# Kernel optimization log

Measured on AMD Instinct MI355X. Metric: run time of the kernel, lower is better.

## Reference

```python
import jax, jax.numpy as jnp
import numpy as np

N_CLASSES = 5
N_SAMPLES = 512
D_EMB = 512


def setup_inputs() -> dict:
    key = jax.random.key(0)
    k1, k2, k3 = jax.random.split(key, 3)
    prediction = jax.random.normal(k1, (N_SAMPLES, D_EMB), dtype=jnp.float32)
    target = jax.random.randint(k2, (N_SAMPLES,), 0, N_CLASSES)
    # learnable_map=None -> all learnable, init = inverse_softplus(0.5 + 0.5*U[0,1))
    t = 0.5 + 0.5 * jax.random.uniform(k3, (N_CLASSES - 1,), dtype=jnp.float32)
    distances_raw = jnp.log(jnp.exp(t) - 1.0)  # inverse softplus (t < 20 always)
    return {"prediction": prediction, "distances_raw": distances_raw, "target": target}


def reference(prediction, distances_raw, target):
    n = prediction.shape[0]
    eps = 1e-8  # torch F.cosine_similarity eps
    xn = prediction / jnp.maximum(jnp.linalg.norm(prediction, axis=1, keepdims=True), eps)
    cos = xn @ xn.T  # [i, j] pairwise cosine similarity

    same = target[:, None] == target[None, :]          # label_diff <= 0
    positives = same & ~jnp.eye(n, dtype=bool)          # same label, not self
    negatives = ~same                                   # different label

    # ordinal class positions from softplus-parameterized gaps
    pos_d = jax.nn.softplus(distances_raw)
    class_pos = jnp.concatenate([jnp.zeros(1, dtype=pos_d.dtype), jnp.cumsum(pos_d)])
    cp = class_pos[target]
    margins = jnp.where(negatives, jnp.abs(cp[:, None] - cp[None, :]), 0.0)  # [i, j]

    # Original loop over anchor-positive columns k:
    #   n_pair_loss[k][i, j] = -cos[i, k] + cos[i, j] + margins[i, j]
    #   valid iff positives[i, k] and negatives[i, j]; invalid -> relu(-inf)=0
    base = cos + margins                                # [i, j]
    diff = base[:, None, :] - cos[:, :, None]           # [i, k, j]
    val = jnp.where(negatives[:, None, :], jax.nn.relu(diff), 0.0)
    s = jnp.where(positives, val.sum(axis=2), 0.0)      # [i, k]
    negcount = negatives.sum(axis=1)                    # [i]
    cnt = jnp.where(positives, negcount[:, None], 0)    # loss_mask2
    L = s / jnp.maximum(cnt, 1)                         # per (anchor i, positive k)

    # mean over nonzero entries (mean_n_pair_loss[mean_n_pair_loss != 0].mean())
    nz = (L != 0.0).sum()
    return L.sum() / jnp.maximum(nz, 1).astype(L.dtype)
```

## Files before the change

### kernel.cpp

```cpp
#include <hip/hip_runtime.h>
#include <math.h>

#define NS 512
#define DE 512
#define NCL 5
#define NBLK 256


__global__ __launch_bounds__(512, 2) void k_gram(const float* __restrict__ pred,
                                                 float* __restrict__ cosmat) {
    const int b  = blockIdx.x;
    const int ga = b >> 2;
    const int q  = b & 3;
    const int a0 = ga * 8;
    const int j0 = q * 128;

    const int tid  = threadIdx.x;
    const int w    = tid >> 6, lane = tid & 63;
    const int g    = lane >> 5;
    const int s    = lane & 31;

    const float4* p4 = (const float4*)pred;

    float4 fr[8][4];
#pragma unroll
    for (int a = 0; a < 8; a++) {
        const float4* pa = p4 + (size_t)(a0 + a) * (DE / 4);
#pragma unroll
        for (int p = 0; p < 4; p++) fr[a][p] = pa[p * 32 + s];
    }

    float rnA[8];
#pragma unroll
    for (int a = 0; a < 8; a++) {
        float aS = 0.0f;
#pragma unroll
        for (int p = 0; p < 4; p++) {
            float4 x = fr[a][p];
            aS = fmaf(x.x, x.x, aS); aS = fmaf(x.y, x.y, aS);
            aS = fmaf(x.z, x.z, aS); aS = fmaf(x.w, x.w, aS);
        }
#pragma unroll
        for (int m = 1; m <= 16; m <<= 1) aS += __shfl_xor(aS, m);
        rnA[a] = 1.0f / fmaxf(sqrtf(aS), 1e-8f);
    }

    const float4* rj0 = p4 + (size_t)(j0 + w * 16 + g) * (DE / 4);
    const int rstep = 2 * (DE / 4);
    float4 x0[4], x1[4];
#pragma unroll
    for (int p = 0; p < 4; p++) x0[p] = rj0[p * 32 + s];
#pragma unroll
    for (int p = 0; p < 4; p++) x1[p] = rj0[rstep + p * 32 + s];

#pragma unroll
    for (int t = 0; t < 8; t++) {
        float4 xn[4];
        if (t < 6) {
            const float4* rjn = rj0 + (size_t)(t + 2) * rstep;
#pragma unroll
            for (int p = 0; p < 4; p++) xn[p] = rjn[p * 32 + s];
        }
        float acc[9];
#pragma unroll
        for (int a = 0; a < 9; a++) acc[a] = 0.0f;
#pragma unroll
        for (int p = 0; p < 4; p++) {
            float4 x = x0[p];
            acc[8] = fmaf(x.x, x.x, acc[8]); acc[8] = fmaf(x.y, x.y, acc[8]);
            acc[8] = fmaf(x.z, x.z, acc[8]); acc[8] = fmaf(x.w, x.w, acc[8]);
#pragma unroll
            for (int a = 0; a < 8; a++) {
                float4 f = fr[a][p];
                acc[a] = fmaf(x.x, f.x, acc[a]); acc[a] = fmaf(x.y, f.y, acc[a]);
                acc[a] = fmaf(x.z, f.z, acc[a]); acc[a] = fmaf(x.w, f.w, acc[a]);
            }
        }
#pragma unroll
        for (int m = 1; m <= 16; m <<= 1) {
#pragma unroll
            for (int a = 0; a < 9; a++) acc[a] += __shfl_xor(acc[a], m);
        }
        if (s == 0) {
            const int jj = j0 + w * 16 + t * 2 + g;
            const float rnj = 1.0f / fmaxf(sqrtf(acc[8]), 1e-8f);
#pragma unroll
            for (int a = 0; a < 8; a++)
                cosmat[(size_t)(a0 + a) * NS + jj] = acc[a] * rnA[a] * rnj;
        }
#pragma unroll
        for (int p = 0; p < 4; p++) { x0[p] = x1[p]; x1[p] = xn[p]; }
    }
}

__global__ __launch_bounds__(512, 2) void k_loss(const float* __restrict__ cosmat,
                                                 const int* __restrict__ target,
                                                 const float* __restrict__ draw,
                                                 float* __restrict__ psum,
                                                 int* __restrict__ pnz) {
    const int b = blockIdx.x;
    const int tid = threadIdx.x;
    const int iA = b, iB = b + 256;

    __shared__ float  ckA[NS], ckB[NS];
    __shared__ float4 v4sA[NS / 4], v4sB[NS / 4];
    __shared__ int    pkA[NS], pkB[NS];
    __shared__ float  spart[NS * 17];
    __shared__ float  wf[8];
    __shared__ int    wi[8];
    __shared__ unsigned int pcA, pcB;

    if (tid == 0) { pcA = 0u; pcB = 0u; }

    const int j = tid;
    const float cA = cosmat[(size_t)iA * NS + j];
    const float cB = cosmat[(size_t)iB * NS + j];

    float cp[NCL];
    cp[0] = 0.0f;
#pragma unroll
    for (int c = 0; c < NCL - 1; c++) cp[c + 1] = cp[c] + log1pf(expf(draw[c]));
    const int tiA = target[iA], tiB = target[iB];
    const float cpA = cp[tiA], cpB = cp[tiB];
    const int tj = target[j];
    const float cpj = cp[tj];
    __syncthreads();

    int nc;
    {
        bool n0 = (tj != tiA);
        ckA[j] = cA;
        ((float*)v4sA)[j] = n0 ? (cA + fabsf(cpA - cpj)) : -1e30f;
        if (!n0 && j != iA) pkA[atomicAdd(&pcA, 1u)] = j;
        nc = (n0 ? 1 : 0);
    }
    {
        bool n0 = (tj != tiB);
        ckB[j] = cB;
        ((float*)v4sB)[j] = n0 ? (cB + fabsf(cpB - cpj)) : -1e30f;
        if (!n0 && j != iB) pkB[atomicAdd(&pcB, 1u)] = j;
        nc += (n0 ? 1 : 0) << 16;
    }
#pragma unroll
    for (int m = 1; m <= 32; m <<= 1) nc += __shfl_xor(nc, m);
    if ((tid & 63) == 0) wi[tid >> 6] = nc;
    __syncthreads();
    int negpack = 0;
#pragma unroll
    for (int q = 0; q < 8; q++) negpack += wi[q];
    const int negA = negpack & 0xffff;
    const int negB = negpack >> 16;
    const unsigned int nposA = pcA, nposB = pcB;

    const int kl = tid & 31, jc = tid >> 5;
    const float denA = (float)(negA > 1 ? negA : 1);
    const float denB = (float)(negB > 1 ? negB : 1);
    float contrib = 0.0f;
    int nzc = 0;

    {
        float4 vj[8];
#pragma unroll
        for (int t = 0; t < 8; t++) vj[t] = v4sA[jc * 8 + t];
        for (unsigned int p = kl; p < nposA; p += 32) {
            const float ckp = ckA[pkA[p]];
            float s0 = 0.0f, s1 = 0.0f;
#pragma unroll
            for (int t = 0; t < 8; t++) {
                float4 wv = vj[t];
                s0 += fmaxf(wv.x - ckp, 0.0f) + fmaxf(wv.y - ckp, 0.0f);
                s1 += fmaxf(wv.z - ckp, 0.0f) + fmaxf(wv.w - ckp, 0.0f);
            }
            spart[p * 17 + jc] = s0 + s1;
        }
        __syncthreads();
        for (unsigned int p = tid; p < nposA; p += 512) {
            float s0 = 0.0f;
#pragma unroll
            for (int q = 0; q < 16; q++) s0 += spart[p * 17 + q];
            contrib += s0 / denA;
            if (s0 != 0.0f) nzc++;
        }
        __syncthreads();
    }
    {
        float4 vj[8];
#pragma unroll
        for (int t = 0; t < 8; t++) vj[t] = v4sB[jc * 8 + t];
        for (unsigned int p = kl; p < nposB; p += 32) {
            const float ckp = ckB[pkB[p]];
            float s0 = 0.0f, s1 = 0.0f;
#pragma unroll
            for (int t = 0; t < 8; t++) {
                float4 wv = vj[t];
                s0 += fmaxf(wv.x - ckp, 0.0f) + fmaxf(wv.y - ckp, 0.0f);
                s1 += fmaxf(wv.z - ckp, 0.0f) + fmaxf(wv.w - ckp, 0.0f);
            }
            spart[p * 17 + jc] = s0 + s1;
        }
        __syncthreads();
        for (unsigned int p = tid; p < nposB; p += 512) {
            float s0 = 0.0f;
#pragma unroll
            for (int q = 0; q < 16; q++) s0 += spart[p * 17 + q];
            contrib += s0 / denB;
            if (s0 != 0.0f) nzc++;
        }
    }

#pragma unroll
    for (int m = 1; m <= 32; m <<= 1) {
        contrib += __shfl_xor(contrib, m);
        nzc     += __shfl_xor(nzc, m);
    }
    __syncthreads();
    if ((tid & 63) == 0) { wf[tid >> 6] = contrib; wi[tid >> 6] = nzc; }
    __syncthreads();
    if (tid == 0) {
        float sfin = 0.0f; int nfin = 0;
#pragma unroll
        for (int q = 0; q < 8; q++) { sfin += wf[q]; nfin += wi[q]; }
        psum[b] = sfin;
        pnz[b]  = nfin;
    }
}

__global__ __launch_bounds__(256) void k_final(const float* __restrict__ psum,
                                               const int* __restrict__ pnz,
                                               float* __restrict__ out) {
    const int tid = threadIdx.x;
    __shared__ float rf[256];
    __shared__ int   ri[256];
    rf[tid] = psum[tid];
    ri[tid] = pnz[tid];
    __syncthreads();
    for (int s = 128; s > 0; s >>= 1) {
        if (tid < s) { rf[tid] += rf[tid + s]; ri[tid] += ri[tid + s]; }
        __syncthreads();
    }
    if (tid == 0) {
        int n = ri[0];
        out[0] = rf[0] / (float)(n > 1 ? n : 1);
    }
}

extern "C" void kernel_launch(void* const* d_in, const int* in_sizes, int n_in,
                              void* d_out, int out_size, void* d_ws, size_t ws_size,
                              hipStream_t stream) {
    const float* pred   = (const float*)d_in[0];
    const float* draw   = (const float*)d_in[1];
    const int*   target = (const int*)d_in[2];
    float* out = (float*)d_out;

    float* cosmat = (float*)d_ws;
    float* psum   = cosmat + (size_t)NS * NS;
    int*   pnz    = (int*)(psum + NBLK);

    hipLaunchKernelGGL(k_gram, dim3(NBLK), dim3(512), 0, stream, pred, cosmat);
    hipLaunchKernelGGL(k_loss, dim3(NBLK), dim3(512), 0, stream,
                       cosmat, target, draw, psum, pnz);
    hipLaunchKernelGGL(k_final, dim3(1), dim3(256), 0, stream, psum, pnz, out);
}
```

Baseline: 81.78 us.

## Fuse gram, loss and final reduction into one cooperative kernel with grid syncs

Merges the three kernel launches (Gram matrix, per-anchor loss, final reduction) into a single cooperative launch, separated by grid-wide barriers. The aim is to remove launch overhead and inter-kernel gaps. In exchange it adds the cost of two grid syncs, and launch bounds drop to one block per CU, which may reduce occupancy or limit register allocation. Block 0 performs the final reduction, reusing shared buffers.

```diff
diff --git a/kernel.cpp b/kernel.cpp
--- a/kernel.cpp
+++ b/kernel.cpp
@@ -1,5 +1,8 @@
 #include <hip/hip_runtime.h>
+#include <hip/hip_cooperative_groups.h>
 #include <math.h>
+
+namespace cg = cooperative_groups;
 
 #define NS 512
 #define DE 512
@@ -7,100 +10,15 @@
 #define NBLK 256
 
 
-__global__ __launch_bounds__(512, 2) void k_gram(const float* __restrict__ pred,
-                                                 float* __restrict__ cosmat) {
-    const int b  = blockIdx.x;
-    const int ga = b >> 2;
-    const int q  = b & 3;
-    const int a0 = ga * 8;
-    const int j0 = q * 128;
-
-    const int tid  = threadIdx.x;
-    const int w    = tid >> 6, lane = tid & 63;
-    const int g    = lane >> 5;
-    const int s    = lane & 31;
-
-    const float4* p4 = (const float4*)pred;
-
-    float4 fr[8][4];
-#pragma unroll
-    for (int a = 0; a < 8; a++) {
-        const float4* pa = p4 + (size_t)(a0 + a) * (DE / 4);
-#pragma unroll
-        for (int p = 0; p < 4; p++) fr[a][p] = pa[p * 32 + s];
-    }
-
-    float rnA[8];
-#pragma unroll
-    for (int a = 0; a < 8; a++) {
-        float aS = 0.0f;
-#pragma unroll
-        for (int p = 0; p < 4; p++) {
-            float4 x = fr[a][p];
-            aS = fmaf(x.x, x.x, aS); aS = fmaf(x.y, x.y, aS);
-            aS = fmaf(x.z, x.z, aS); aS = fmaf(x.w, x.w, aS);
-        }
-#pragma unroll
-        for (int m = 1; m <= 16; m <<= 1) aS += __shfl_xor(aS, m);
-        rnA[a] = 1.0f / fmaxf(sqrtf(aS), 1e-8f);
-    }
-
-    const float4* rj0 = p4 + (size_t)(j0 + w * 16 + g) * (DE / 4);
-    const int rstep = 2 * (DE / 4);
-    float4 x0[4], x1[4];
-#pragma unroll
-    for (int p = 0; p < 4; p++) x0[p] = rj0[p * 32 + s];
-#pragma unroll
-    for (int p = 0; p < 4; p++) x1[p] = rj0[rstep + p * 32 + s];
-
-#pragma unroll
-    for (int t = 0; t < 8; t++) {
-        float4 xn[4];
-        if (t < 6) {
-            const float4* rjn = rj0 + (size_t)(t + 2) * rstep;
-#pragma unroll
-            for (int p = 0; p < 4; p++) xn[p] = rjn[p * 32 + s];
-        }
-        float acc[9];
-#pragma unroll
-        for (int a = 0; a < 9; a++) acc[a] = 0.0f;
-#pragma unroll
-        for (int p = 0; p < 4; p++) {
-            float4 x = x0[p];
-            acc[8] = fmaf(x.x, x.x, acc[8]); acc[8] = fmaf(x.y, x.y, acc[8]);
-            acc[8] = fmaf(x.z, x.z, acc[8]); acc[8] = fmaf(x.w, x.w, acc[8]);
-#pragma unroll
-            for (int a = 0; a < 8; a++) {
-                float4 f = fr[a][p];
-                acc[a] = fmaf(x.x, f.x, acc[a]); acc[a] = fmaf(x.y, f.y, acc[a]);
-                acc[a] = fmaf(x.z, f.z, acc[a]); acc[a] = fmaf(x.w, f.w, acc[a]);
-            }
-        }
-#pragma unroll
-        for (int m = 1; m <= 16; m <<= 1) {
-#pragma unroll
-            for (int a = 0; a < 9; a++) acc[a] += __shfl_xor(acc[a], m);
-        }
-        if (s == 0) {
-            const int jj = j0 + w * 16 + t * 2 + g;
-            const float rnj = 1.0f / fmaxf(sqrtf(acc[8]), 1e-8f);
-#pragma unroll
-            for (int a = 0; a < 8; a++)
-                cosmat[(size_t)(a0 + a) * NS + jj] = acc[a] * rnA[a] * rnj;
-        }
-#pragma unroll
-        for (int p = 0; p < 4; p++) { x0[p] = x1[p]; x1[p] = xn[p]; }
-    }
-}
-
-__global__ __launch_bounds__(512, 2) void k_loss(const float* __restrict__ cosmat,
+__global__ __launch_bounds__(512, 1) void k_coop(const float* __restrict__ pred,
                                                  const int* __restrict__ target,
                                                  const float* __restrict__ draw,
+                                                 float* __restrict__ cosmat,
                                                  float* __restrict__ psum,
-                                                 int* __restrict__ pnz) {
+                                                 int* __restrict__ pnz,
+                                                 float* __restrict__ out) {
     const int b = blockIdx.x;
     const int tid = threadIdx.x;
-    const int iA = b, iB = b + 256;
 
     __shared__ float  ckA[NS], ckB[NS];
     __shared__ float4 v4sA[NS / 4], v4sB[NS / 4];
@@ -110,137 +28,221 @@
     __shared__ int    wi[8];
     __shared__ unsigned int pcA, pcB;
 
-    if (tid == 0) { pcA = 0u; pcB = 0u; }
-
-    const int j = tid;
-    const float cA = cosmat[(size_t)iA * NS + j];
-    const float cB = cosmat[(size_t)iB * NS + j];
-
-    float cp[NCL];
-    cp[0] = 0.0f;
-#pragma unroll
-    for (int c = 0; c < NCL - 1; c++) cp[c + 1] = cp[c] + log1pf(expf(draw[c]));
-    const int tiA = target[iA], tiB = target[iB];
-    const float cpA = cp[tiA], cpB = cp[tiB];
-    const int tj = target[j];
-    const float cpj = cp[tj];
-    __syncthreads();
-
-    int nc;
     {
-        bool n0 = (tj != tiA);
-        ckA[j] = cA;
-        ((float*)v4sA)[j] = n0 ? (cA + fabsf(cpA - cpj)) : -1e30f;
-        if (!n0 && j != iA) pkA[atomicAdd(&pcA, 1u)] = j;
-        nc = (n0 ? 1 : 0);
+        const int ga = b >> 2;
+        const int q  = b & 3;
+        const int a0 = ga * 8;
+        const int j0 = q * 128;
+
+        const int w    = tid >> 6, lane = tid & 63;
+        const int g    = lane >> 5;
+        const int s    = lane & 31;
+
+        const float4* p4 = (const float4*)pred;
+
+        float4 fr[8][4];
+#pragma unroll
+        for (int a = 0; a < 8; a++) {
+            const float4* pa = p4 + (size_t)(a0 + a) * (DE / 4);
+#pragma unroll
+            for (int p = 0; p < 4; p++) fr[a][p] = pa[p * 32 + s];
+        }
+
+        float rnA[8];
+#pragma unroll
+        for (int a = 0; a < 8; a++) {
+            float aS = 0.0f;
+#pragma unroll
+            for (int p = 0; p < 4; p++) {
+                float4 x = fr[a][p];
+                aS = fmaf(x.x, x.x, aS); aS = fmaf(x.y, x.y, aS);
+                aS = fmaf(x.z, x.z, aS); aS = fmaf(x.w, x.w, aS);
+            }
+#pragma unroll
+            for (int m = 1; m <= 16; m <<= 1) aS += __shfl_xor(aS, m);
+            rnA[a] = 1.0f / fmaxf(sqrtf(aS), 1e-8f);
+        }
+
+        const float4* rj0 = p4 + (size_t)(j0 + w * 16 + g) * (DE / 4);
+        const int rstep = 2 * (DE / 4);
+        float4 x0[4], x1[4];
+#pragma unroll
+        for (int p = 0; p < 4; p++) x0[p] = rj0[p * 32 + s];
+#pragma unroll
+        for (int p = 0; p < 4; p++) x1[p] = rj0[rstep + p * 32 + s];
+
+#pragma unroll
+        for (int t = 0; t < 8; t++) {
+            float4 xn[4];
+            if (t < 6) {
+                const float4* rjn = rj0 + (size_t)(t + 2) * rstep;
+#pragma unroll
+                for (int p = 0; p < 4; p++) xn[p] = rjn[p * 32 + s];
+            }
+            float acc[9];
+#pragma unroll
+            for (int a = 0; a < 9; a++) acc[a] = 0.0f;
+#pragma unroll
+            for (int p = 0; p < 4; p++) {
+                float4 x = x0[p];
+                acc[8] = fmaf(x.x, x.x, acc[8]); acc[8] = fmaf(x.y, x.y, acc[8]);
+                acc[8] = fmaf(x.z, x.z, acc[8]); acc[8] = fmaf(x.w, x.w, acc[8]);
+#pragma unroll
+                for (int a = 0; a < 8; a++) {
+                    float4 f = fr[a][p];
+                    acc[a] = fmaf(x.x, f.x, acc[a]); acc[a] = fmaf(x.y, f.y, acc[a]);
+                    acc[a] = fmaf(x.z, f.z, acc[a]); acc[a] = fmaf(x.w, f.w, acc[a]);
+                }
+            }
+#pragma unroll
+            for (int m = 1; m <= 16; m <<= 1) {
+#pragma unroll
+                for (int a = 0; a < 9; a++) acc[a] += __shfl_xor(acc[a], m);
+            }
+            if (s == 0) {
+                const int jj = j0 + w * 16 + t * 2 + g;
+                const float rnj = 1.0f / fmaxf(sqrtf(acc[8]), 1e-8f);
+#pragma unroll
+                for (int a = 0; a < 8; a++)
+                    cosmat[(size_t)(a0 + a) * NS + jj] = acc[a] * rnA[a] * rnj;
+            }
+#pragma unroll
+            for (int p = 0; p < 4; p++) { x0[p] = x1[p]; x1[p] = xn[p]; }
+        }
     }
+
+    cg::this_grid().sync();
+
     {
-        bool n0 = (tj != tiB);
-        ckB[j] = cB;
-        ((float*)v4sB)[j] = n0 ? (cB + fabsf(cpB - cpj)) : -1e30f;
-        if (!n0 && j != iB) pkB[atomicAdd(&pcB, 1u)] = j;
-        nc += (n0 ? 1 : 0) << 16;
+        const int iA = b, iB = b + 256;
+        if (tid == 0) { pcA = 0u; pcB = 0u; }
+
+        const int j = tid;
+        const float cA = cosmat[(size_t)iA * NS + j];
+        const float cB = cosmat[(size_t)iB * NS + j];
+
+        float cp[NCL];
+        cp[0] = 0.0f;
+#pragma unroll
+        for (int c = 0; c < NCL - 1; c++) cp[c + 1] = cp[c] + log1pf(expf(draw[c]));
+        const int tiA = target[iA], tiB = target[iB];
+        const float cpA = cp[tiA], cpB = cp[tiB];
+        const int tj = target[j];
+        const float cpj = cp[tj];
+        __syncthreads();
+
+        int nc;
+        {
+            bool n0 = (tj != tiA);
+            ckA[j] = cA;
+            ((float*)v4sA)[j] = n0 ? (cA + fabsf(cpA - cpj)) : -1e30f;
+            if (!n0 && j != iA) pkA[atomicAdd(&pcA, 1u)] = j;
+            nc = (n0 ? 1 : 0);
+        }
+        {
+            bool n0 = (tj != tiB);
+            ckB[j] = cB;
+            ((float*)v4sB)[j] = n0 ? (cB + fabsf(cpB - cpj)) : -1e30f;
+            if (!n0 && j != iB) pkB[atomicAdd(&pcB, 1u)] = j;
+            nc += (n0 ? 1 : 0) << 16;
+        }
+#pragma unroll
+        for (int m = 1; m <= 32; m <<= 1) nc += __shfl_xor(nc, m);
+        if ((tid & 63) == 0) wi[tid >> 6] = nc;
+        __syncthreads();
+        int negpack = 0;
+#pragma unroll
+        for (int q = 0; q < 8; q++) negpack += wi[q];
+        const int negA = negpack & 0xffff;
+        const int negB = negpack >> 16;
+        const unsigned int nposA = pcA, nposB = pcB;
+
+        const int kl = tid & 31, jc = tid >> 5;
+        const float denA = (float)(negA > 1 ? negA : 1);
+        const float denB = (float)(negB > 1 ? negB : 1);
+        float contrib = 0.0f;
+        int nzc = 0;
+
+        {
+            float4 vj[8];
+#pragma unroll
+            for (int t = 0; t < 8; t++) vj[t] = v4sA[jc * 8 + t];
+            for (unsigned int p = kl; p < nposA; p += 32) {
+                const float ckp = ckA[pkA[p]];
+                float s0 = 0.0f, s1 = 0.0f;
+#pragma unroll
+                for (int t = 0; t < 8; t++) {
+                    float4 wv = vj[t];
+                    s0 += fmaxf(wv.x - ckp, 0.0f) + fmaxf(wv.y - ckp, 0.0f);
+                    s1 += fmaxf(wv.z - ckp, 0.0f) + fmaxf(wv.w - ckp, 0.0f);
+                }
+                spart[p * 17 + jc] = s0 + s1;
+            }
+            __syncthreads();
+            for (unsigned int p = tid; p < nposA; p += 512) {
+                float s0 = 0.0f;
+#pragma unroll
+                for (int q = 0; q < 16; q++) s0 += spart[p * 17 + q];
+                contrib += s0 / denA;
+                if (s0 != 0.0f) nzc++;
+            }
+            __syncthreads();
+        }
+        {
+            float4 vj[8];
+#pragma unroll
+            for (int t = 0; t < 8; t++) vj[t] = v4sB[jc * 8 + t];
+            for (unsigned int p = kl; p < nposB; p += 32) {
+                const float ckp = ckB[pkB[p]];
+                float s0 = 0.0f, s1 = 0.0f;
+#pragma unroll
+                for (int t = 0; t < 8; t++) {
+                    float4 wv = vj[t];
+                    s0 += fmaxf(wv.x - ckp, 0.0f) + fmaxf(wv.y - ckp, 0.0f);
+                    s1 += fmaxf(wv.z - ckp, 0.0f) + fmaxf(wv.w - ckp, 0.0f);
+                }
+                spart[p * 17 + jc] = s0 + s1;
+            }
+            __syncthreads();
+            for (unsigned int p = tid; p < nposB; p += 512) {
+                float s0 = 0.0f;
+#pragma unroll
+                for (int q = 0; q < 16; q++) s0 += spart[p * 17 + q];
+                contrib += s0 / denB;
+                if (s0 != 0.0f) nzc++;
+            }
+        }
+
+#pragma unroll
+        for (int m = 1; m <= 32; m <<= 1) {
+            contrib += __shfl_xor(contrib, m);
+            nzc     += __shfl_xor(nzc, m);
+        }
+        __syncthreads();
+        if ((tid & 63) == 0) { wf[tid >> 6] = contrib; wi[tid >> 6] = nzc; }
+        __syncthreads();
+        if (tid == 0) {
+            float sfin = 0.0f; int nfin = 0;
+#pragma unroll
+            for (int q = 0; q < 8; q++) { sfin += wf[q]; nfin += wi[q]; }
+            psum[b] = sfin;
+            pnz[b]  = nfin;
+        }
     }
-#pragma unroll
-    for (int m = 1; m <= 32; m <<= 1) nc += __shfl_xor(nc, m);
-    if ((tid & 63) == 0) wi[tid >> 6] = nc;
-    __syncthreads();
-    int negpack = 0;
-#pragma unroll
-    for (int q = 0; q < 8; q++) negpack += wi[q];
-    const int negA = negpack & 0xffff;
-    const int negB = negpack >> 16;
-    const unsigned int nposA = pcA, nposB = pcB;
-
-    const int kl = tid & 31, jc = tid >> 5;
-    const float denA = (float)(negA > 1 ? negA : 1);
-    const float denB = (float)(negB > 1 ? negB : 1);
-    float contrib = 0.0f;
-    int nzc = 0;
-
-    {
-        float4 vj[8];
-#pragma unroll
-        for (int t = 0; t < 8; t++) vj[t] = v4sA[jc * 8 + t];
-        for (unsigned int p = kl; p < nposA; p += 32) {
-            const float ckp = ckA[pkA[p]];
-            float s0 = 0.0f, s1 = 0.0f;
-#pragma unroll
-            for (int t = 0; t < 8; t++) {
-                float4 wv = vj[t];
-                s0 += fmaxf(wv.x - ckp, 0.0f) + fmaxf(wv.y - ckp, 0.0f);
-                s1 += fmaxf(wv.z - ckp, 0.0f) + fmaxf(wv.w - ckp, 0.0f);
-            }
-            spart[p * 17 + jc] = s0 + s1;
-        }
-        __syncthreads();
-        for (unsigned int p = tid; p < nposA; p += 512) {
-            float s0 = 0.0f;
-#pragma unroll
-            for (int q = 0; q < 16; q++) s0 += spart[p * 17 + q];
-            contrib += s0 / denA;
-            if (s0 != 0.0f) nzc++;
-        }
-        __syncthreads();
-    }
-    {
-        float4 vj[8];
-#pragma unroll
-        for (int t = 0; t < 8; t++) vj[t] = v4sB[jc * 8 + t];
-        for (unsigned int p = kl; p < nposB; p += 32) {
-            const float ckp = ckB[pkB[p]];
-            float s0 = 0.0f, s1 = 0.0f;
-#pragma unroll
-            for (int t = 0; t < 8; t++) {
-                float4 wv = vj[t];
-                s0 += fmaxf(wv.x - ckp, 0.0f) + fmaxf(wv.y - ckp, 0.0f);
-                s1 += fmaxf(wv.z - ckp, 0.0f) + fmaxf(wv.w - ckp, 0.0f);
-            }
-            spart[p * 17 + jc] = s0 + s1;
-        }
-        __syncthreads();
-        for (unsigned int p = tid; p < nposB; p += 512) {
-            float s0 = 0.0f;
-#pragma unroll
-            for (int q = 0; q < 16; q++) s0 += spart[p * 17 + q];
-            contrib += s0 / denB;
-            if (s0 != 0.0f) nzc++;
-        }
-    }
-
-#pragma unroll
-    for (int m = 1; m <= 32; m <<= 1) {
-        contrib += __shfl_xor(contrib, m);
-        nzc     += __shfl_xor(nzc, m);
-    }
-    __syncthreads();
-    if ((tid & 63) == 0) { wf[tid >> 6] = contrib; wi[tid >> 6] = nzc; }
-    __syncthreads();
-    if (tid == 0) {
-        float sfin = 0.0f; int nfin = 0;
-#pragma unroll
-        for (int q = 0; q < 8; q++) { sfin += wf[q]; nfin += wi[q]; }
-        psum[b] = sfin;
-        pnz[b]  = nfin;
-    }
-}
-
-__global__ __launch_bounds__(256) void k_final(const float* __restrict__ psum,
-                                               const int* __restrict__ pnz,
-                                               float* __restrict__ out) {
-    const int tid = threadIdx.x;
-    __shared__ float rf[256];
-    __shared__ int   ri[256];
-    rf[tid] = psum[tid];
-    ri[tid] = pnz[tid];
-    __syncthreads();
-    for (int s = 128; s > 0; s >>= 1) {
-        if (tid < s) { rf[tid] += rf[tid + s]; ri[tid] += ri[tid + s]; }
-        __syncthreads();
-    }
-    if (tid == 0) {
-        int n = ri[0];
-        out[0] = rf[0] / (float)(n > 1 ? n : 1);
+
+    cg::this_grid().sync();
+
+    if (b == 0) {
+        if (tid < NBLK) { ckA[tid] = psum[tid]; pkA[tid] = pnz[tid]; }
+        __syncthreads();
+        for (int st = NBLK / 2; st > 0; st >>= 1) {
+            if (tid < st) { ckA[tid] += ckA[tid + st]; pkA[tid] += pkA[tid + st]; }
+            __syncthreads();
+        }
+        if (tid == 0) {
+            int n = pkA[0];
+            out[0] = ckA[0] / (float)(n > 1 ? n : 1);
+        }
     }
 }
 
@@ -256,8 +258,8 @@
     float* psum   = cosmat + (size_t)NS * NS;
     int*   pnz    = (int*)(psum + NBLK);
 
-    hipLaunchKernelGGL(k_gram, dim3(NBLK), dim3(512), 0, stream, pred, cosmat);
-    hipLaunchKernelGGL(k_loss, dim3(NBLK), dim3(512), 0, stream,
-                       cosmat, target, draw, psum, pnz);
-    hipLaunchKernelGGL(k_final, dim3(1), dim3(256), 0, stream, psum, pnz, out);
+    void* args[] = {(void*)&pred, (void*)&target, (void*)&draw,
+                    (void*)&cosmat, (void*)&psum, (void*)&pnz, (void*)&out};
+    hipLaunchCooperativeKernel((void*)k_coop, dim3(NBLK), dim3(512),
+                               args, 0, stream);
 }
```

Result: slower. 144.9 us (+77.2%).
